# Performance work log

Hardware: AMD Instinct MI355X
Metric: run time of the kernel (lower is better)

## Reference

```python
import jax, jax.numpy as jnp
import numpy as np

SIZE = 1024
N_HEAD = 16
HEAD_DIM = SIZE // N_HEAD


def setup_inputs() -> dict:
    key = jax.random.key(0)
    ks = jax.random.split(key, 5)
    s = 1.0 / np.sqrt(SIZE)
    return {
        "x": jax.random.normal(ks[0], (4, 2048, SIZE), dtype=jnp.float32),
        "w_qkv": jax.random.uniform(ks[1], (SIZE, 3 * SIZE), dtype=jnp.float32, minval=-s, maxval=s),
        "b_qkv": jax.random.uniform(ks[2], (3 * SIZE,), dtype=jnp.float32, minval=-s, maxval=s),
        "w_fc": jax.random.uniform(ks[3], (SIZE, SIZE), dtype=jnp.float32, minval=-s, maxval=s),
        "b_fc": jax.random.uniform(ks[4], (SIZE,), dtype=jnp.float32, minval=-s, maxval=s),
    }


def reference(x, w_qkv, b_qkv, w_fc, b_fc):
    B, S, D = x.shape
    qkv = x @ w_qkv + b_qkv                      # [B, S, 3D]
    qkv = qkv.reshape(B, S, 3, N_HEAD, HEAD_DIM)
    qkv = jnp.transpose(qkv, (2, 0, 3, 1, 4))    # [3, B, H, S, hd]
    q, k, v = qkv[0], qkv[1], qkv[2]
    scale = 1.0 / np.sqrt(HEAD_DIM).astype(np.float32)
    scores = jnp.einsum('bhqd,bhkd->bhqk', q, k) * scale
    attn = jax.nn.softmax(scores, axis=-1)
    out = jnp.einsum('bhqk,bhkd->bhqd', attn, v)  # [B, H, S, hd]
    out = jnp.transpose(out, (0, 2, 1, 3)).reshape(B, S, D)
    return out @ w_fc + b_fc
```

## Files before the change

### kernel.cpp

```cpp
#include <hip/hip_runtime.h>

#define DEV __device__ __forceinline__

typedef float  f32x4   __attribute__((ext_vector_type(4)));
typedef float  f32x16  __attribute__((ext_vector_type(16)));
typedef short  s16x4   __attribute__((ext_vector_type(4)));
typedef short  short8  __attribute__((ext_vector_type(8)));
typedef __bf16 bf16x8  __attribute__((ext_vector_type(8)));
typedef unsigned u32x2 __attribute__((ext_vector_type(2)));
typedef unsigned u32x4 __attribute__((ext_vector_type(4)));

DEV f32x4 mfma_bf16(short8 a, short8 b, f32x4 c) {
    return __builtin_amdgcn_mfma_f32_16x16x32_bf16(
        __builtin_bit_cast(bf16x8, a), __builtin_bit_cast(bf16x8, b), c, 0, 0, 0);
}

DEV f32x16 mfma32(short8 a, short8 b, f32x16 c) {
    return __builtin_amdgcn_mfma_f32_32x32x16_bf16(
        __builtin_bit_cast(bf16x8, a), __builtin_bit_cast(bf16x8, b), c, 0, 0, 0);
}

DEV void gload_lds16(const void* g, void* l) {
    __builtin_amdgcn_global_load_lds(
        (const __attribute__((address_space(1))) unsigned int*)g,
        (__attribute__((address_space(3))) unsigned int*)l, 16, 0, 0);
}

DEV short f2bf(float f) { return __builtin_bit_cast(short, (__bf16)f); }

DEV unsigned cvt_pk_bf16(float lo, float hi) {
    unsigned r;
    asm("v_cvt_pk_bf16_f32 %0, %1, %2" : "=v"(r) : "v"(lo), "v"(hi));
    return r;
}

DEV u32x2 pl32swap(unsigned a, unsigned b) {
    return __builtin_amdgcn_permlane32_swap(a, b, false, false);
}

DEV int xcd_swz(int fid, int nwg) {
    int cpx = nwg >> 3;
    return (fid & 7) * cpx + (fid >> 3);
}

__global__ void cast_x(const float* __restrict__ in, unsigned short* __restrict__ out, int n) {
    int i = (blockIdx.x * 256 + threadIdx.x) * 8;
    if (i >= n) return;
    f32x4 a = *(const f32x4*)(in + i);
    f32x4 b = *(const f32x4*)(in + i + 4);
    short8 o;
    o[0] = f2bf(a[0]); o[1] = f2bf(a[1]); o[2] = f2bf(a[2]); o[3] = f2bf(a[3]);
    o[4] = f2bf(b[0]); o[5] = f2bf(b[1]); o[6] = f2bf(b[2]); o[7] = f2bf(b[3]);
    *(short8*)(out + i) = o;
}

__global__ void transpose_cast2(const float* __restrict__ wqkv, unsigned short* __restrict__ oq,
                                const float* __restrict__ wfc, unsigned short* __restrict__ of) {
    __shared__ float tile[64][65];
    int bid = blockIdx.x;
    const float* in;
    unsigned short* out;
    int bx, by, C;
    if (bid < 48 * 16) {
        in = wqkv; out = oq; C = 3072;
        bx = bid % 48; by = bid / 48;
    } else {
        bid -= 48 * 16;
        in = wfc; out = of; C = 1024;
        bx = bid % 16; by = bid / 16;
    }
    const int R = 1024;
    int c0 = bx * 64, r0 = by * 64;
    int tx = threadIdx.x & 63, ty = threadIdx.x >> 6;
#pragma unroll
    for (int i = 0; i < 16; i++) {
        int r = i * 4 + ty;
        tile[r][tx] = in[(size_t)(r0 + r) * C + c0 + tx];
    }
    __syncthreads();
#pragma unroll
    for (int i = 0; i < 16; i++) {
        int cc = i * 4 + ty;
        out[(size_t)(c0 + cc) * R + r0 + tx] = (unsigned short)f2bf(tile[tx][cc]);
    }
}

template <int MODE>
__global__ __launch_bounds__(256, 2) void gemm_bt(
    const unsigned short* __restrict__ A, const unsigned short* __restrict__ Bt,
    const float* __restrict__ bias, float* __restrict__ out_f32,
    unsigned short* __restrict__ q_out, unsigned short* __restrict__ k_out,
    unsigned short* __restrict__ v_out, int K) {
    __shared__ __align__(16) char smem[65536];
    const int t = threadIdx.x;
    const int lane = t & 63, w = t >> 6;
    const int wr = w >> 1, wc = w & 1;
    const int nbx = gridDim.x;
    const int sw = xcd_swz(blockIdx.y * nbx + blockIdx.x, nbx * gridDim.y);
    const int rowBase = (sw / nbx) * 128, colBase = (sw % nbx) * 128;

#define STAGE_AB(k0, buf)                                                           \
    do {                                                                            \
        char* lA_ = smem + (buf) * 32768;                                           \
        char* lB_ = lA_ + 16384;                                                    \
        _Pragma("unroll")                                                           \
        for (int i_ = 0; i_ < 4; i_++) {                                            \
            int c_ = i_ * 256 + t;                                                  \
            int r_ = c_ >> 3, j_ = c_ & 7;                                          \
            int jj_ = j_ ^ (r_ & 7);                                                \
            gload_lds16(A  + (size_t)(rowBase + r_) * K + (k0) + jj_ * 8,           \
                        lA_ + c_ * 16);                                             \
            gload_lds16(Bt + (size_t)(colBase + r_) * K + (k0) + jj_ * 8,           \
                        lB_ + c_ * 16);                                             \
        }                                                                           \
    } while (0)

    STAGE_AB(0, 0);

    f32x4 acc[4][4] = {};
    int cur = 0;

    for (int k0 = 0; k0 < K; k0 += 64) {
        __syncthreads();
        if (k0 + 64 < K) STAGE_AB(k0 + 64, cur ^ 1);
        char* lA = smem + cur * 32768;
        char* lB = lA + 16384;
#pragma unroll
        for (int ks = 0; ks < 2; ks++) {
            const int colb = (ks * 4 + (lane >> 4)) * 16;
            short8 af[4], bfr[4];
#pragma unroll
            for (int m2 = 0; m2 < 4; m2++) {
                int r = wr * 64 + m2 * 16 + (lane & 15);
                af[m2] = *(const short8*)(lA + r * 128 + (colb ^ ((r & 7) << 4)));
            }
#pragma unroll
            for (int n2 = 0; n2 < 4; n2++) {
                int r = wc * 64 + n2 * 16 + (lane & 15);
                bfr[n2] = *(const short8*)(lB + r * 128 + (colb ^ ((r & 7) << 4)));
            }
            __builtin_amdgcn_s_setprio(1);
#pragma unroll
            for (int m2 = 0; m2 < 4; m2++)
#pragma unroll
                for (int n2 = 0; n2 < 4; n2++)
                    acc[m2][n2] = mfma_bf16(af[m2], bfr[n2], acc[m2][n2]);
            __builtin_amdgcn_s_setprio(0);
        }
        cur ^= 1;
    }
#undef STAGE_AB

    if (MODE == 0) {
        const int which = colBase >> 10;
        if (which == 2) {
#pragma unroll
            for (int n2 = 0; n2 < 4; n2++) {
                int gc = colBase + wc * 64 + n2 * 16 + (lane & 15);
                int rem = gc & 1023;
                int h = rem >> 6, d = rem & 63;
                float bv = bias[gc];
#pragma unroll
                for (int m2 = 0; m2 < 4; m2++) {
                    int grb = rowBase + wr * 64 + m2 * 16 + ((lane >> 4) << 2);
                    int b = grb >> 11, s = grb & 2047;
                    s16x4 o;
#pragma unroll
                    for (int r2 = 0; r2 < 4; r2++) o[r2] = f2bf(acc[m2][n2][r2] + bv);
                    *(s16x4*)(v_out + ((size_t)((b * 16 + h) * 64 + d)) * 2048 + s) = o;
                }
            }
        } else {
            const float qs = which == 0 ? 0.18033688011112042f : 1.0f;
            unsigned short* dst = which == 0 ? q_out : k_out;
#pragma unroll
            for (int n2 = 0; n2 < 4; n2++) {
                int gc = colBase + wc * 64 + n2 * 16 + (lane & 15);
                int rem = gc & 1023;
                int h = rem >> 6, d = rem & 63;
                float bv = bias[gc];
#pragma unroll
                for (int m2 = 0; m2 < 4; m2++) {
                    int grb = rowBase + wr * 64 + m2 * 16 + ((lane >> 4) << 2);
#pragma unroll
                    for (int r2 = 0; r2 < 4; r2++) {
                        int gr = grb + r2;
                        int b = gr >> 11, s = gr & 2047;
                        float v = (acc[m2][n2][r2] + bv) * qs;
                        dst[((size_t)((b * 16 + h) * 2048 + s)) * 64 + d] =
                            (unsigned short)f2bf(v);
                    }
                }
            }
        }
    } else {
#pragma unroll
        for (int n2 = 0; n2 < 4; n2++) {
            int gc = colBase + wc * 64 + n2 * 16 + (lane & 15);
            float bv = bias[gc];
#pragma unroll
            for (int m2 = 0; m2 < 4; m2++) {
                int grb = rowBase + wr * 64 + m2 * 16 + ((lane >> 4) << 2);
#pragma unroll
                for (int r2 = 0; r2 < 4; r2++)
                    out_f32[(size_t)(grb + r2) * 1024 + gc] = acc[m2][n2][r2] + bv;
            }
        }
    }
}

__global__ __launch_bounds__(256, 4) void fattn(
    const unsigned short* __restrict__ Qb, const unsigned short* __restrict__ Kb,
    const unsigned short* __restrict__ Vt, unsigned short* __restrict__ O) {
    __shared__ __align__(16) char smem[32768];
    const int t = threadIdx.x, lane = t & 63, w = t >> 6;
    const int h = lane >> 5, l5 = lane & 31;
    const int sw = xcd_swz(blockIdx.x, 1024);
    const int bh = sw >> 4;
    const int q0 = (sw & 15) * 128 + w * 32;
    const size_t slab = (size_t)bh * 2048 * 64;

    short8 qf[4];
#pragma unroll
    for (int s = 0; s < 4; s++)
        qf[s] = *(const short8*)(Qb + slab + (size_t)(q0 + l5) * 64 + s * 16 + h * 8);

#define STAGE_KV(kv0, buf)                                                          \
    do {                                                                            \
        char* dK_ = smem + (buf) * 8192;                                            \
        char* dV_ = smem + 16384 + (buf) * 8192;                                    \
        _Pragma("unroll")                                                           \
        for (int i_ = 0; i_ < 2; i_++) {                                            \
            int c_ = i_ * 256 + t, r_ = c_ >> 3, j_ = c_ & 7, jj_ = j_ ^ (r_ & 7);  \
            gload_lds16(Kb + slab + (size_t)((kv0) + r_) * 64 + jj_ * 8,            \
                        dK_ + c_ * 16);                                             \
            gload_lds16(Vt + slab + (size_t)r_ * 2048 + (kv0) + jj_ * 8,            \
                        dV_ + c_ * 16);                                             \
        }                                                                           \
    } while (0)

    STAGE_KV(0, 0);

    f32x4 lsum4 = {};
    f32x16 accO0 = {}, accO1 = {};

    int cur = 0;
    for (int kt = 0; kt < 32; kt++) {
        __syncthreads();
        if (kt < 31) STAGE_KV((kt + 1) * 64, cur ^ 1);
        char* lKc = smem + cur * 8192;
        char* lVc = smem + 16384 + cur * 8192;

        f32x16 st0 = {}, st1 = {};
        __builtin_amdgcn_s_setprio(1);
#pragma unroll
        for (int s = 0; s < 4; s++) {
            const int cb = s * 32 + h * 16;
            short8 k0 = *(const short8*)(lKc + l5 * 128 + (cb ^ ((l5 & 7) << 4)));
            short8 k1 = *(const short8*)(lKc + (32 + l5) * 128 + (cb ^ ((l5 & 7) << 4)));
            st0 = mfma32(k0, qf[s], st0);
            st1 = mfma32(k1, qf[s], st1);
        }
        __builtin_amdgcn_s_setprio(0);

#pragma unroll
        for (int kv2 = 0; kv2 < 2; kv2++) {
            const f32x16 stc = kv2 ? st1 : st0;
            unsigned pk[8];
#pragma unroll
            for (int i = 0; i < 8; i++) {
                float p0 = __builtin_amdgcn_exp2f(stc[2 * i]);
                float p1 = __builtin_amdgcn_exp2f(stc[2 * i + 1]);
                lsum4[i & 3] += p0 + p1;
                pk[i] = cvt_pk_bf16(p0, p1);
            }
            u32x2 s02 = pl32swap(pk[0], pk[2]);
            u32x2 s13 = pl32swap(pk[1], pk[3]);
            u32x2 s46 = pl32swap(pk[4], pk[6]);
            u32x2 s57 = pl32swap(pk[5], pk[7]);
            u32x4 af0 = {s02[0], s13[0], s02[1], s13[1]};
            u32x4 af1 = {s46[0], s57[0], s46[1], s57[1]};
            __builtin_amdgcn_s_setprio(1);
#pragma unroll
            for (int s = 0; s < 2; s++) {
                short8 ap = __builtin_bit_cast(short8, s == 0 ? af0 : af1);
                const int cb = kv2 * 64 + s * 32 + h * 16;
                short8 v0 = *(const short8*)(lVc + l5 * 128 + (cb ^ ((l5 & 7) << 4)));
                short8 v1 = *(const short8*)(lVc + (32 + l5) * 128 + (cb ^ ((l5 & 7) << 4)));
                accO0 = mfma32(ap, v0, accO0);
                accO1 = mfma32(ap, v1, accO1);
            }
            __builtin_amdgcn_s_setprio(0);
        }
        cur ^= 1;
    }
#undef STAGE_KV

    float lsum = lsum4[0] + lsum4[1] + lsum4[2] + lsum4[3];
    lsum += __shfl_xor(lsum, 32);
    float inv = 1.f / lsum;

    const int b = bh >> 4, hh = bh & 15;
#pragma unroll
    for (int r = 0; r < 16; r++) {
        int row = (r & 3) + 8 * (r >> 2) + 4 * h;
        float iv = __shfl(inv, row, 64);
        size_t base = ((size_t)(b * 2048 + q0 + row)) * 1024 + hh * 64;
        O[base + l5]      = (unsigned short)f2bf(accO0[r] * iv);
        O[base + 32 + l5] = (unsigned short)f2bf(accO1[r] * iv);
    }
}

extern "C" void kernel_launch(void* const* d_in, const int* in_sizes, int n_in,
                              void* d_out, int out_size, void* d_ws, size_t ws_size,
                              hipStream_t stream) {
    const float* x     = (const float*)d_in[0];
    const float* w_qkv = (const float*)d_in[1];
    const float* b_qkv = (const float*)d_in[2];
    const float* w_fc  = (const float*)d_in[3];
    const float* b_fc  = (const float*)d_in[4];

    char* ws = (char*)d_ws;
    unsigned short* Xb    = (unsigned short*)(ws);
    unsigned short* WqkvT = (unsigned short*)(ws + 16777216);
    unsigned short* WfcT  = (unsigned short*)(ws + 23068672);
    unsigned short* Qb    = (unsigned short*)(ws + 25165824);
    unsigned short* Kb    = (unsigned short*)(ws + 41943040);
    unsigned short* Vt    = (unsigned short*)(ws + 58720256);
    unsigned short* Ao    = (unsigned short*)(ws + 75497472);

    cast_x<<<dim3(8388608 / (256 * 8)), 256, 0, stream>>>(x, Xb, 8388608);
    transpose_cast2<<<dim3(48 * 16 + 16 * 16), 256, 0, stream>>>(w_qkv, WqkvT, w_fc, WfcT);

    gemm_bt<0><<<dim3(3072 / 128, 8192 / 128), 256, 0, stream>>>(
        Xb, WqkvT, b_qkv, nullptr, Qb, Kb, Vt, 1024);

    fattn<<<dim3(1024), 256, 0, stream>>>(Qb, Kb, Vt, Ao);

    gemm_bt<1><<<dim3(1024 / 128, 8192 / 128), 256, 0, stream>>>(
        Ao, WfcT, b_fc, (float*)d_out, nullptr, nullptr, nullptr, 1024);
}
```

Baseline: 253.2 us.

## Fuse prep kernels and double attention block size to share K/V tiles

Merges the x cast and weight transpose-cast kernels into one launch, removing a kernel launch boundary. Attention blocks now use 512 threads (8 waves) covering 256 queries, so each staged K/V tile in LDS is shared by twice as many waves. Each thread now issues one load per K/V tile instead of two. Grid halves to 512 blocks, which lowers block-level parallelism and may reduce occupancy with the 512-thread launch bound.

```diff
diff --git a/kernel.cpp b/kernel.cpp
--- a/kernel.cpp
+++ b/kernel.cpp
@@ -43,29 +43,30 @@
     return (fid & 7) * cpx + (fid >> 3);
 }
 
-__global__ void cast_x(const float* __restrict__ in, unsigned short* __restrict__ out, int n) {
-    int i = (blockIdx.x * 256 + threadIdx.x) * 8;
-    if (i >= n) return;
-    f32x4 a = *(const f32x4*)(in + i);
-    f32x4 b = *(const f32x4*)(in + i + 4);
-    short8 o;
-    o[0] = f2bf(a[0]); o[1] = f2bf(a[1]); o[2] = f2bf(a[2]); o[3] = f2bf(a[3]);
-    o[4] = f2bf(b[0]); o[5] = f2bf(b[1]); o[6] = f2bf(b[2]); o[7] = f2bf(b[3]);
-    *(short8*)(out + i) = o;
-}
-
-__global__ void transpose_cast2(const float* __restrict__ wqkv, unsigned short* __restrict__ oq,
-                                const float* __restrict__ wfc, unsigned short* __restrict__ of) {
+__global__ void prep_fused(const float* __restrict__ x, unsigned short* __restrict__ xb,
+                           const float* __restrict__ wqkv, unsigned short* __restrict__ oq,
+                           const float* __restrict__ wfc, unsigned short* __restrict__ of) {
+    int bid = blockIdx.x;
+    if (bid < 4096) {
+        int i = (bid * 256 + threadIdx.x) * 8;
+        f32x4 a = *(const f32x4*)(x + i);
+        f32x4 b = *(const f32x4*)(x + i + 4);
+        short8 o;
+        o[0] = f2bf(a[0]); o[1] = f2bf(a[1]); o[2] = f2bf(a[2]); o[3] = f2bf(a[3]);
+        o[4] = f2bf(b[0]); o[5] = f2bf(b[1]); o[6] = f2bf(b[2]); o[7] = f2bf(b[3]);
+        *(short8*)(xb + i) = o;
+        return;
+    }
     __shared__ float tile[64][65];
-    int bid = blockIdx.x;
     const float* in;
     unsigned short* out;
     int bx, by, C;
-    if (bid < 48 * 16) {
+    if (bid < 4096 + 768) {
+        bid -= 4096;
         in = wqkv; out = oq; C = 3072;
         bx = bid % 48; by = bid / 48;
     } else {
-        bid -= 48 * 16;
+        bid -= 4096 + 768;
         in = wfc; out = of; C = 1024;
         bx = bid % 16; by = bid / 16;
     }
@@ -209,15 +210,15 @@
     }
 }
 
-__global__ __launch_bounds__(256, 4) void fattn(
+__global__ __launch_bounds__(512, 4) void fattn(
     const unsigned short* __restrict__ Qb, const unsigned short* __restrict__ Kb,
     const unsigned short* __restrict__ Vt, unsigned short* __restrict__ O) {
     __shared__ __align__(16) char smem[32768];
     const int t = threadIdx.x, lane = t & 63, w = t >> 6;
     const int h = lane >> 5, l5 = lane & 31;
-    const int sw = xcd_swz(blockIdx.x, 1024);
-    const int bh = sw >> 4;
-    const int q0 = (sw & 15) * 128 + w * 32;
+    const int sw = xcd_swz(blockIdx.x, 512);
+    const int bh = sw >> 3;
+    const int q0 = (sw & 7) * 256 + w * 32;
     const size_t slab = (size_t)bh * 2048 * 64;
 
     short8 qf[4];
@@ -229,14 +230,9 @@
     do {                                                                            \
         char* dK_ = smem + (buf) * 8192;                                            \
         char* dV_ = smem + 16384 + (buf) * 8192;                                    \
-        _Pragma("unroll")                                                           \
-        for (int i_ = 0; i_ < 2; i_++) {                                            \
-            int c_ = i_ * 256 + t, r_ = c_ >> 3, j_ = c_ & 7, jj_ = j_ ^ (r_ & 7);  \
-            gload_lds16(Kb + slab + (size_t)((kv0) + r_) * 64 + jj_ * 8,            \
-                        dK_ + c_ * 16);                                             \
-            gload_lds16(Vt + slab + (size_t)r_ * 2048 + (kv0) + jj_ * 8,            \
-                        dV_ + c_ * 16);                                             \
-        }                                                                           \
+        int r_ = t >> 3, j_ = t & 7, jj_ = j_ ^ (r_ & 7);                           \
+        gload_lds16(Kb + slab + (size_t)((kv0) + r_) * 64 + jj_ * 8, dK_ + t * 16); \
+        gload_lds16(Vt + slab + (size_t)r_ * 2048 + (kv0) + jj_ * 8, dV_ + t * 16); \
     } while (0)
 
     STAGE_KV(0, 0);
@@ -329,13 +325,12 @@
     unsigned short* Vt    = (unsigned short*)(ws + 58720256);
     unsigned short* Ao    = (unsigned short*)(ws + 75497472);
 
-    cast_x<<<dim3(8388608 / (256 * 8)), 256, 0, stream>>>(x, Xb, 8388608);
-    transpose_cast2<<<dim3(48 * 16 + 16 * 16), 256, 0, stream>>>(w_qkv, WqkvT, w_fc, WfcT);
+    prep_fused<<<dim3(4096 + 768 + 256), 256, 0, stream>>>(x, Xb, w_qkv, WqkvT, w_fc, WfcT);
 
     gemm_bt<0><<<dim3(3072 / 128, 8192 / 128), 256, 0, stream>>>(
         Xb, WqkvT, b_qkv, nullptr, Qb, Kb, Vt, 1024);
 
-    fattn<<<dim3(1024), 256, 0, stream>>>(Qb, Kb, Vt, Ao);
+    fattn<<<dim3(512), 512, 0, stream>>>(Qb, Kb, Vt, Ao);
 
     gemm_bt<1><<<dim3(1024 / 128, 8192 / 128), 256, 0, stream>>>(
         Ao, WfcT, b_fc, (float*)d_out, nullptr, nullptr, nullptr, 1024);
```

New measurement: 256.8 us. Within noise of the previous version (+1.4%).
